# Kernel optimization log

Hardware: AMD Instinct MI355X
Metric: run time of the kernel (lower is better)

## Reference

```python
import jax, jax.numpy as jnp
import numpy as np

D_MODEL = 2048
N_HEADS = 16
D_HEAD = 128
D_LATENT = 512


def setup_inputs() -> dict:
    key = jax.random.key(0)
    ks = jax.random.split(key, 5)
    s = lambda fan_in: 1.0 / np.sqrt(fan_in)
    x = jax.random.normal(ks[0], (2, 2048, D_MODEL), dtype=jnp.float32)
    # nn.Linear weights stored as [out, in]; we keep [in, out] for x @ W
    W_q = jax.random.uniform(ks[1], (D_MODEL, N_HEADS * D_HEAD), jnp.float32, -s(D_MODEL), s(D_MODEL))
    W_kv_down = jax.random.uniform(ks[2], (D_MODEL, D_LATENT), jnp.float32, -s(D_MODEL), s(D_MODEL))
    W_kv_up = jax.random.uniform(ks[3], (D_LATENT, N_HEADS * D_HEAD), jnp.float32, -s(D_LATENT), s(D_LATENT))
    W_o = jax.random.uniform(ks[4], (N_HEADS * D_HEAD, D_MODEL), jnp.float32, -s(N_HEADS * D_HEAD), s(N_HEADS * D_HEAD))
    return {"x": x, "W_q": W_q, "W_kv_down": W_kv_down, "W_kv_up": W_kv_up, "W_o": W_o}


def reference(x, W_q, W_kv_down, W_kv_up, W_o):
    B, S, _ = x.shape
    # q: [B, H, S, Dh]
    q = (x @ W_q).reshape(B, S, N_HEADS, D_HEAD).transpose(0, 2, 1, 3)
    # latent compression then up-projection; shared K = V
    latent = x @ W_kv_down                      # [B, S, Dl]
    kv = (latent @ W_kv_up).reshape(B, S, N_HEADS, D_HEAD).transpose(0, 2, 1, 3)
    scale = 1.0 / np.sqrt(D_HEAD).astype(np.float32)
    scores = jnp.einsum('bhqd,bhkd->bhqk', q, kv) * scale  # [B,H,S,S]
    probs = jax.nn.softmax(scores, axis=-1)
    out = jnp.einsum('bhqk,bhkd->bhqd', probs, kv)          # [B,H,S,Dh]
    out = out.transpose(0, 2, 1, 3).reshape(B, S, N_HEADS * D_HEAD)
    return out @ W_o
```

## Files before the change

kernel.cpp:

```cpp
#include <hip/hip_runtime.h>

typedef __attribute__((ext_vector_type(8))) __bf16 bf16x8;
typedef __attribute__((ext_vector_type(4))) float f32x4;
typedef __attribute__((ext_vector_type(8))) unsigned short u16x8;
typedef __attribute__((ext_vector_type(4))) unsigned short u16x4;

#define MFMA16(a, b, c) __builtin_amdgcn_mfma_f32_16x16x32_bf16((a), (b), (c), 0, 0, 0)

__device__ __forceinline__ unsigned short f2bf(float f) {
    unsigned int u = __float_as_uint(f);
    unsigned int r = (u + 0x7FFFu + ((u >> 16) & 1u)) >> 16;
    return (unsigned short)r;
}

__global__ __launch_bounds__(256) void k_convert(const float* __restrict__ in,
                                                 unsigned short* __restrict__ out, int n4) {
    int i = blockIdx.x * 256 + threadIdx.x;
    if (i >= n4) return;
    const float4 v = ((const float4*)in)[i];
    u16x4 o = { f2bf(v.x), f2bf(v.y), f2bf(v.z), f2bf(v.w) };
    ((u16x4*)out)[i] = o;
}

__global__ __launch_bounds__(256) void k_transpose(const float* __restrict__ in,
                                                   unsigned short* __restrict__ out,
                                                   int R, int C) {
    __shared__ float tile[32][33];
    const int tx = threadIdx.x & 31, ty = threadIdx.x >> 5;
    const int c0 = blockIdx.x * 32, r0 = blockIdx.y * 32;
#pragma unroll
    for (int i = 0; i < 4; ++i)
        tile[ty + i * 8][tx] = in[(size_t)(r0 + ty + i * 8) * C + c0 + tx];
    __syncthreads();
#pragma unroll
    for (int i = 0; i < 4; ++i)
        out[(size_t)(c0 + ty + i * 8) * R + r0 + tx] = f2bf(tile[tx][ty + i * 8]);
}

template <int OUT_MODE>
__global__ __launch_bounds__(256) void k_gemm_bt(const unsigned short* __restrict__ A,
                                                 const unsigned short* __restrict__ B,
                                                 void* __restrict__ Cv,
                                                 unsigned short* __restrict__ Ct,
                                                 int M, int N, int K, float alpha) {
    __shared__ alignas(16) unsigned short As[128 * 32];
    __shared__ alignas(16) unsigned short Bs[128 * 32];
    const int tid = threadIdx.x;
    const int wave = tid >> 6;
    const int lane = tid & 63;
    const int l16 = lane & 15;
    const int quad = lane >> 4;
    const int bm = blockIdx.y * 128;
    const int bn = blockIdx.x * 128;
    const int wm = (wave >> 1) * 64;
    const int wn = (wave & 1) * 64;

    const f32x4 fzero = {0.f, 0.f, 0.f, 0.f};
    f32x4 acc[4][4];
#pragma unroll
    for (int i = 0; i < 4; ++i)
#pragma unroll
        for (int j = 0; j < 4; ++j) acc[i][j] = fzero;

    auto AsL = (__attribute__((address_space(3))) unsigned short*)As;
    auto BsL = (__attribute__((address_space(3))) unsigned short*)Bs;

    const int c0 = wave * 128 + lane;

    for (int kt = 0; kt < K; kt += 32) {
        __syncthreads();
#pragma unroll
        for (int j = 0; j < 2; ++j) {
            const int c = c0 + j * 64;
            __builtin_amdgcn_global_load_lds(
                (const __attribute__((address_space(1))) void*)(A + (size_t)(bm + (c >> 2)) * K + kt + (c & 3) * 8),
                (__attribute__((address_space(3))) void*)(AsL + c * 8), 16, 0, 0);
            __builtin_amdgcn_global_load_lds(
                (const __attribute__((address_space(1))) void*)(B + (size_t)(bn + (c >> 2)) * K + kt + (c & 3) * 8),
                (__attribute__((address_space(3))) void*)(BsL + c * 8), 16, 0, 0);
        }
        __syncthreads();

        bf16x8 af[4], bfr[4];
#pragma unroll
        for (int mt = 0; mt < 4; ++mt)
            af[mt] = *(const bf16x8*)(As + (wm + mt * 16 + l16) * 32 + quad * 8);
#pragma unroll
        for (int nt = 0; nt < 4; ++nt)
            bfr[nt] = *(const bf16x8*)(Bs + (wn + nt * 16 + l16) * 32 + quad * 8);
#pragma unroll
        for (int mt = 0; mt < 4; ++mt)
#pragma unroll
            for (int nt = 0; nt < 4; ++nt)
                acc[mt][nt] = MFMA16(af[mt], bfr[nt], acc[mt][nt]);
    }

#pragma unroll
    for (int mt = 0; mt < 4; ++mt)
#pragma unroll
        for (int nt = 0; nt < 4; ++nt) {
            const int row0 = bm + wm + mt * 16 + quad * 4;
            const int col = bn + wn + nt * 16 + l16;
            u16x4 pk;
#pragma unroll
            for (int r = 0; r < 4; ++r) {
                const float v0 = acc[mt][nt][r];
                if (OUT_MODE == 0) {
                    ((float*)Cv)[(size_t)(row0 + r) * N + col] = v0 * alpha;
                } else if (OUT_MODE == 3) {
                    if (col < 2048)
                        ((unsigned short*)Cv)[(size_t)(row0 + r) * 2048 + col] = f2bf(v0 * alpha);
                    else
                        Ct[(size_t)(row0 + r) * 512 + (col - 2048)] = f2bf(v0);
                } else {
                    const unsigned short b = f2bf(v0 * alpha);
                    ((unsigned short*)Cv)[(size_t)(row0 + r) * N + col] = b;
                    pk[r] = b;
                }
            }
            if (OUT_MODE == 2) {
                const size_t ti =
                    ((size_t)((row0 >> 11) * (N >> 7) + (col >> 7)) * 128 + (col & 127)) * 2048 +
                    (row0 & 2047);
                *(u16x4*)(Ct + ti) = pk;
            }
        }
}

__global__ __launch_bounds__(256, 2) void k_attn(const unsigned short* __restrict__ Q,
                                                 const unsigned short* __restrict__ KV,
                                                 const unsigned short* __restrict__ KVT,
                                                 unsigned short* __restrict__ O) {
    __shared__ alignas(16) unsigned short Ks[64 * 128];
    __shared__ alignas(16) unsigned short Vt[128 * 64];
    __shared__ alignas(16) unsigned short Ps[4 * 32 * 64];

    const int tid = threadIdx.x;
    const int wave = tid >> 6, lane = tid & 63;
    const int l16 = lane & 15, quad = lane >> 4;
    const int l8 = l16 & 7;
    const int qt = blockIdx.x;
    const int bh = blockIdx.y;
    const size_t tokbase = (size_t)(bh >> 4) * 2048;
    const int hcol = (bh & 15) * 128;
    const unsigned short* kvt_head = KVT + (size_t)bh * (128 * 2048);

    bf16x8 qf[2][4];
    const int qrow0 = qt * 128 + wave * 32;
#pragma unroll
    for (int nt = 0; nt < 2; ++nt) {
        const unsigned short* qp =
            Q + (tokbase + qrow0 + nt * 16 + l16) * 2048 + hcol + quad * 8;
#pragma unroll
        for (int kd = 0; kd < 4; ++kd) qf[nt][kd] = *(const bf16x8*)(qp + kd * 32);
    }

    const f32x4 fzero = {0.f, 0.f, 0.f, 0.f};
    f32x4 o_acc[8][2];
#pragma unroll
    for (int dt = 0; dt < 8; ++dt)
#pragma unroll
        for (int nt = 0; nt < 2; ++nt) o_acc[dt][nt] = fzero;
    float l_i[2] = {0.f, 0.f};

    const int krow = tid >> 4, kchunk = tid & 15;
    const int vrow = tid >> 3, vchunk = tid & 7;

    unsigned short* Pw = Ps + wave * (32 * 64);

    for (int kt = 0; kt < 32; ++kt) {
        __syncthreads();
#pragma unroll
        for (int p = 0; p < 4; ++p) {
            const int r = p * 16 + krow;
            const u16x8 v =
                *(const u16x8*)(KV + (tokbase + kt * 64 + r) * 2048 + hcol + kchunk * 8);
            const int sw = (kchunk & 8) | ((kchunk & 7) ^ (r & 7));
            *(u16x8*)(Ks + r * 128 + sw * 8) = v;
        }
#pragma unroll
        for (int p = 0; p < 4; ++p) {
            const int d = p * 32 + vrow;
            const u16x8 v = *(const u16x8*)(kvt_head + d * 2048 + kt * 64 + vchunk * 8);
            const int sw = vchunk ^ (d & 7);
            *(u16x8*)(Vt + d * 64 + sw * 8) = v;
        }
        __syncthreads();

        f32x4 st[4][2];
#pragma unroll
        for (int mt = 0; mt < 4; ++mt)
#pragma unroll
            for (int nt = 0; nt < 2; ++nt) st[mt][nt] = fzero;
#pragma unroll
        for (int kd = 0; kd < 4; ++kd)
#pragma unroll
            for (int mt = 0; mt < 4; ++mt) {
                const int c = kd * 4 + quad;
                const int sw = (c & 8) | ((c & 7) ^ l8);
                const bf16x8 kf = *(const bf16x8*)(Ks + (mt * 16 + l16) * 128 + sw * 8);
                st[mt][0] = MFMA16(kf, qf[0][kd], st[mt][0]);
                st[mt][1] = MFMA16(kf, qf[1][kd], st[mt][1]);
            }

#pragma unroll
        for (int nt = 0; nt < 2; ++nt) {
            float rs = 0.f;
            unsigned short* prow = Pw + (nt * 16 + l16) * 64;
#pragma unroll
            for (int mt = 0; mt < 4; ++mt) {
                u16x4 pk;
#pragma unroll
                for (int r = 0; r < 4; ++r) {
                    const float p = __expf(st[mt][nt][r]);
                    rs += p;
                    pk[r] = f2bf(p);
                }
                const int c = mt * 2 + (quad >> 1);
                *(u16x4*)(prow + (c ^ l8) * 8 + (quad & 1) * 4) = pk;
            }
            rs += __shfl_xor(rs, 16);
            rs += __shfl_xor(rs, 32);
            l_i[nt] += rs;
        }

        __builtin_amdgcn_sched_barrier(0);

#pragma unroll
        for (int s = 0; s < 2; ++s) {
            const int c = s * 4 + quad;
            const int sw = (c ^ l8) * 8;
            bf16x8 pfr[2];
#pragma unroll
            for (int nt = 0; nt < 2; ++nt)
                pfr[nt] = *(const bf16x8*)(Pw + (nt * 16 + l16) * 64 + sw);
#pragma unroll
            for (int dt = 0; dt < 8; ++dt) {
                const bf16x8 vf = *(const bf16x8*)(Vt + (dt * 16 + l16) * 64 + sw);
                o_acc[dt][0] = MFMA16(vf, pfr[0], o_acc[dt][0]);
                o_acc[dt][1] = MFMA16(vf, pfr[1], o_acc[dt][1]);
            }
        }
    }

#pragma unroll
    for (int nt = 0; nt < 2; ++nt) {
        const float inv = 1.0f / l_i[nt];
        unsigned short* dst = O + (tokbase + qrow0 + nt * 16 + l16) * 2048 + hcol;
#pragma unroll
        for (int dt = 0; dt < 8; ++dt) {
            u16x4 pk;
#pragma unroll
            for (int r = 0; r < 4; ++r) pk[r] = f2bf(o_acc[dt][nt][r] * inv);
            *(u16x4*)(dst + dt * 16 + quad * 4) = pk;
        }
    }
}

extern "C" void kernel_launch(void* const* d_in, const int* in_sizes, int n_in,
                              void* d_out, int out_size, void* d_ws, size_t ws_size,
                              hipStream_t stream) {
    const float* x = (const float*)d_in[0];
    const float* W_q = (const float*)d_in[1];
    const float* W_kvd = (const float*)d_in[2];
    const float* W_kvu = (const float*)d_in[3];
    const float* W_o = (const float*)d_in[4];

    char* w = (char*)d_ws;
    unsigned short* xb = (unsigned short*)(w);
    unsigned short* kvT = xb;
    unsigned short* qb = (unsigned short*)(w + (size_t)16 * 1024 * 1024);
    unsigned short* kvb = (unsigned short*)(w + (size_t)32 * 1024 * 1024);
    unsigned short* Wo_t = (unsigned short*)(w + (size_t)48 * 1024 * 1024);
    unsigned short* Wcat_t = (unsigned short*)(w + (size_t)56 * 1024 * 1024);
    unsigned short* Wkvu_t = (unsigned short*)(w + (size_t)66 * 1024 * 1024);
    unsigned short* lat = (unsigned short*)(w + (size_t)68 * 1024 * 1024);

    k_convert<<<8192, 256, 0, stream>>>(x, xb, 2097152);
    k_transpose<<<dim3(64, 64), 256, 0, stream>>>(W_q, Wcat_t, 2048, 2048);
    k_transpose<<<dim3(16, 64), 256, 0, stream>>>(W_kvd, Wcat_t + 2048 * 2048, 2048, 512);
    k_transpose<<<dim3(64, 16), 256, 0, stream>>>(W_kvu, Wkvu_t, 512, 2048);
    k_transpose<<<dim3(64, 64), 256, 0, stream>>>(W_o, Wo_t, 2048, 2048);

    k_gemm_bt<3><<<dim3(20, 32), 256, 0, stream>>>(xb, Wcat_t, qb, lat, 4096, 2560, 2048,
                                                   0.08838834764831845f);
    k_gemm_bt<2><<<dim3(16, 32), 256, 0, stream>>>(lat, Wkvu_t, kvb, kvT, 4096, 2048, 512,
                                                   1.0f);
    k_attn<<<dim3(16, 32), 256, 0, stream>>>(qb, kvb, kvT, qb);
    k_gemm_bt<0><<<dim3(16, 32), 256, 0, stream>>>(qb, Wo_t, d_out, nullptr, 4096, 2048, 2048,
                                                   1.0f);
}
```

Baseline: 347.5 us.

## Fuse prep kernels and double-buffer LDS tiles in GEMM and attention

Merges the bf16 convert and four weight-transpose launches into one prep kernel that dispatches on block index. Double-buffers the shared-memory tiles in the GEMM, issuing the async global-to-LDS load for the next K step before computing the current one. Double-buffers the K/V tiles in attention with a register prefetch two tiles ahead, which drops one barrier per iteration. This aims to hide global memory latency and launch overhead, at the cost of more LDS (attention goes to about 80KB per block, which may limit its 2-block occupancy) and more register pressure.

```diff
diff --git a/kernel.cpp b/kernel.cpp
--- a/kernel.cpp
+++ b/kernel.cpp
@@ -13,21 +13,12 @@
     return (unsigned short)r;
 }
 
-__global__ __launch_bounds__(256) void k_convert(const float* __restrict__ in,
-                                                 unsigned short* __restrict__ out, int n4) {
-    int i = blockIdx.x * 256 + threadIdx.x;
-    if (i >= n4) return;
-    const float4 v = ((const float4*)in)[i];
-    u16x4 o = { f2bf(v.x), f2bf(v.y), f2bf(v.z), f2bf(v.w) };
-    ((u16x4*)out)[i] = o;
-}
-
-__global__ __launch_bounds__(256) void k_transpose(const float* __restrict__ in,
-                                                   unsigned short* __restrict__ out,
-                                                   int R, int C) {
+__device__ __forceinline__ void transpose_tile(const float* __restrict__ in,
+                                               unsigned short* __restrict__ out,
+                                               int R, int C, int bx, int by) {
     __shared__ float tile[32][33];
     const int tx = threadIdx.x & 31, ty = threadIdx.x >> 5;
-    const int c0 = blockIdx.x * 32, r0 = blockIdx.y * 32;
+    const int c0 = bx * 32, r0 = by * 32;
 #pragma unroll
     for (int i = 0; i < 4; ++i)
         tile[ty + i * 8][tx] = in[(size_t)(r0 + ty + i * 8) * C + c0 + tx];
@@ -35,6 +26,36 @@
 #pragma unroll
     for (int i = 0; i < 4; ++i)
         out[(size_t)(c0 + ty + i * 8) * R + r0 + tx] = f2bf(tile[tx][ty + i * 8]);
+}
+
+__global__ __launch_bounds__(256) void k_prep(const float* __restrict__ x,
+                                              const float* __restrict__ Wq,
+                                              const float* __restrict__ Wkvd,
+                                              const float* __restrict__ Wkvu,
+                                              const float* __restrict__ Wo,
+                                              unsigned short* __restrict__ xb,
+                                              unsigned short* __restrict__ Wcat_t,
+                                              unsigned short* __restrict__ Wkvu_t,
+                                              unsigned short* __restrict__ Wo_t) {
+    const int i = blockIdx.x;
+    if (i < 8192) {
+        const int idx = i * 256 + threadIdx.x;
+        const float4 v = ((const float4*)x)[idx];
+        u16x4 o = { f2bf(v.x), f2bf(v.y), f2bf(v.z), f2bf(v.w) };
+        ((u16x4*)xb)[idx] = o;
+    } else if (i < 12288) {
+        const int j = i - 8192;
+        transpose_tile(Wq, Wcat_t, 2048, 2048, j & 63, j >> 6);
+    } else if (i < 13312) {
+        const int j = i - 12288;
+        transpose_tile(Wkvd, Wcat_t + 2048 * 2048, 2048, 512, j & 15, j >> 4);
+    } else if (i < 14336) {
+        const int j = i - 13312;
+        transpose_tile(Wkvu, Wkvu_t, 512, 2048, j & 63, j >> 6);
+    } else {
+        const int j = i - 14336;
+        transpose_tile(Wo, Wo_t, 2048, 2048, j & 63, j >> 6);
+    }
 }
 
 template <int OUT_MODE>
@@ -43,8 +64,8 @@
                                                  void* __restrict__ Cv,
                                                  unsigned short* __restrict__ Ct,
                                                  int M, int N, int K, float alpha) {
-    __shared__ alignas(16) unsigned short As[128 * 32];
-    __shared__ alignas(16) unsigned short Bs[128 * 32];
+    __shared__ alignas(16) unsigned short As[2 * 128 * 32];
+    __shared__ alignas(16) unsigned short Bs[2 * 128 * 32];
     const int tid = threadIdx.x;
     const int wave = tid >> 6;
     const int lane = tid & 63;
@@ -67,27 +88,36 @@
 
     const int c0 = wave * 128 + lane;
 
-    for (int kt = 0; kt < K; kt += 32) {
-        __syncthreads();
+    auto stage = [&](int kt32) {
+        const int boff = (kt32 & 1) * (128 * 32);
+        const int kt = kt32 * 32;
 #pragma unroll
         for (int j = 0; j < 2; ++j) {
             const int c = c0 + j * 64;
             __builtin_amdgcn_global_load_lds(
                 (const __attribute__((address_space(1))) void*)(A + (size_t)(bm + (c >> 2)) * K + kt + (c & 3) * 8),
-                (__attribute__((address_space(3))) void*)(AsL + c * 8), 16, 0, 0);
+                (__attribute__((address_space(3))) void*)(AsL + boff + c * 8), 16, 0, 0);
             __builtin_amdgcn_global_load_lds(
                 (const __attribute__((address_space(1))) void*)(B + (size_t)(bn + (c >> 2)) * K + kt + (c & 3) * 8),
-                (__attribute__((address_space(3))) void*)(BsL + c * 8), 16, 0, 0);
-        }
+                (__attribute__((address_space(3))) void*)(BsL + boff + c * 8), 16, 0, 0);
+        }
+    };
+
+    const int nk = K >> 5;
+    stage(0);
+    for (int kt32 = 0; kt32 < nk; ++kt32) {
         __syncthreads();
+        if (kt32 + 1 < nk) stage(kt32 + 1);
+        const unsigned short* Ab = As + (kt32 & 1) * (128 * 32);
+        const unsigned short* Bb = Bs + (kt32 & 1) * (128 * 32);
 
         bf16x8 af[4], bfr[4];
 #pragma unroll
         for (int mt = 0; mt < 4; ++mt)
-            af[mt] = *(const bf16x8*)(As + (wm + mt * 16 + l16) * 32 + quad * 8);
+            af[mt] = *(const bf16x8*)(Ab + (wm + mt * 16 + l16) * 32 + quad * 8);
 #pragma unroll
         for (int nt = 0; nt < 4; ++nt)
-            bfr[nt] = *(const bf16x8*)(Bs + (wn + nt * 16 + l16) * 32 + quad * 8);
+            bfr[nt] = *(const bf16x8*)(Bb + (wn + nt * 16 + l16) * 32 + quad * 8);
 #pragma unroll
         for (int mt = 0; mt < 4; ++mt)
 #pragma unroll
@@ -131,8 +161,8 @@
                                                  const unsigned short* __restrict__ KV,
                                                  const unsigned short* __restrict__ KVT,
                                                  unsigned short* __restrict__ O) {
-    __shared__ alignas(16) unsigned short Ks[64 * 128];
-    __shared__ alignas(16) unsigned short Vt[128 * 64];
+    __shared__ alignas(16) unsigned short Ks[2 * 64 * 128];
+    __shared__ alignas(16) unsigned short Vt[2 * 128 * 64];
     __shared__ alignas(16) unsigned short Ps[4 * 32 * 64];
 
     const int tid = threadIdx.x;
@@ -168,24 +198,42 @@
 
     unsigned short* Pw = Ps + wave * (32 * 64);
 
+    u16x8 kR[4], vR[4];
+    auto load_tile = [&](int kt) {
+#pragma unroll
+        for (int p = 0; p < 4; ++p) {
+            kR[p] = *(const u16x8*)(KV + (tokbase + kt * 64 + p * 16 + krow) * 2048 +
+                                    hcol + kchunk * 8);
+            vR[p] = *(const u16x8*)(kvt_head + (size_t)(p * 32 + vrow) * 2048 + kt * 64 +
+                                    vchunk * 8);
+        }
+    };
+    auto store_tile = [&](int kt) {
+        unsigned short* Kb = Ks + (kt & 1) * (64 * 128);
+        unsigned short* Vb = Vt + (kt & 1) * (128 * 64);
+#pragma unroll
+        for (int p = 0; p < 4; ++p) {
+            const int r = p * 16 + krow;
+            const int swk = (kchunk & 8) | ((kchunk & 7) ^ (r & 7));
+            *(u16x8*)(Kb + r * 128 + swk * 8) = kR[p];
+            const int d = p * 32 + vrow;
+            const int swv = vchunk ^ (d & 7);
+            *(u16x8*)(Vb + d * 64 + swv * 8) = vR[p];
+        }
+    };
+
+    load_tile(0);
+    store_tile(0);
+    load_tile(1);
+
     for (int kt = 0; kt < 32; ++kt) {
         __syncthreads();
-#pragma unroll
-        for (int p = 0; p < 4; ++p) {
-            const int r = p * 16 + krow;
-            const u16x8 v =
-                *(const u16x8*)(KV + (tokbase + kt * 64 + r) * 2048 + hcol + kchunk * 8);
-            const int sw = (kchunk & 8) | ((kchunk & 7) ^ (r & 7));
-            *(u16x8*)(Ks + r * 128 + sw * 8) = v;
-        }
-#pragma unroll
-        for (int p = 0; p < 4; ++p) {
-            const int d = p * 32 + vrow;
-            const u16x8 v = *(const u16x8*)(kvt_head + d * 2048 + kt * 64 + vchunk * 8);
-            const int sw = vchunk ^ (d & 7);
-            *(u16x8*)(Vt + d * 64 + sw * 8) = v;
-        }
-        __syncthreads();
+        if (kt < 31) {
+            store_tile(kt + 1);
+            if (kt < 30) load_tile(kt + 2);
+        }
+        const unsigned short* Kb = Ks + (kt & 1) * (64 * 128);
+        const unsigned short* Vb = Vt + (kt & 1) * (128 * 64);
 
         f32x4 st[4][2];
 #pragma unroll
@@ -198,7 +246,7 @@
             for (int mt = 0; mt < 4; ++mt) {
                 const int c = kd * 4 + quad;
                 const int sw = (c & 8) | ((c & 7) ^ l8);
-                const bf16x8 kf = *(const bf16x8*)(Ks + (mt * 16 + l16) * 128 + sw * 8);
+                const bf16x8 kf = *(const bf16x8*)(Kb + (mt * 16 + l16) * 128 + sw * 8);
                 st[mt][0] = MFMA16(kf, qf[0][kd], st[mt][0]);
                 st[mt][1] = MFMA16(kf, qf[1][kd], st[mt][1]);
             }
@@ -236,7 +284,7 @@
                 pfr[nt] = *(const bf16x8*)(Pw + (nt * 16 + l16) * 64 + sw);
 #pragma unroll
             for (int dt = 0; dt < 8; ++dt) {
-                const bf16x8 vf = *(const bf16x8*)(Vt + (dt * 16 + l16) * 64 + sw);
+                const bf16x8 vf = *(const bf16x8*)(Vb + (dt * 16 + l16) * 64 + sw);
                 o_acc[dt][0] = MFMA16(vf, pfr[0], o_acc[dt][0]);
                 o_acc[dt][1] = MFMA16(vf, pfr[1], o_acc[dt][1]);
             }
@@ -276,11 +324,7 @@
     unsigned short* Wkvu_t = (unsigned short*)(w + (size_t)66 * 1024 * 1024);
     unsigned short* lat = (unsigned short*)(w + (size_t)68 * 1024 * 1024);
 
-    k_convert<<<8192, 256, 0, stream>>>(x, xb, 2097152);
-    k_transpose<<<dim3(64, 64), 256, 0, stream>>>(W_q, Wcat_t, 2048, 2048);
-    k_transpose<<<dim3(16, 64), 256, 0, stream>>>(W_kvd, Wcat_t + 2048 * 2048, 2048, 512);
-    k_transpose<<<dim3(64, 16), 256, 0, stream>>>(W_kvu, Wkvu_t, 512, 2048);
-    k_transpose<<<dim3(64, 64), 256, 0, stream>>>(W_o, Wo_t, 2048, 2048);
+    k_prep<<<18432, 256, 0, stream>>>(x, W_q, W_kvd, W_kvu, W_o, xb, Wcat_t, Wkvu_t, Wo_t);
 
     k_gemm_bt<3><<<dim3(20, 32), 256, 0, stream>>>(xb, Wcat_t, qb, lat, 4096, 2560, 2048,
                                                    0.08838834764831845f);
```

Measured after the change: 322.2 us. -7.3%, faster.
